# Kernel tuning notes

Measured on AMD Instinct MI355X. Metric: run time of the kernel, lower is better.

The kernel has to match this reference:

```python
import jax, jax.numpy as jnp
import numpy as np

D_MODEL = 1024
N_HEADS = 16
HEAD_DIM = D_MODEL // N_HEADS
ROPE_BASE = 10000.0


def setup_inputs() -> dict:
    key = jax.random.key(0)
    ks = jax.random.split(key, 9)
    s = 0.02
    inp = {
        "x": jax.random.normal(ks[0], (2, 2048, D_MODEL), dtype=jnp.float32),
        "Wq": jax.random.normal(ks[1], (D_MODEL, D_MODEL), dtype=jnp.float32) * s,
        "bq": jnp.zeros((D_MODEL,), dtype=jnp.float32),
        "Wk": jax.random.normal(ks[2], (D_MODEL, D_MODEL), dtype=jnp.float32) * s,
        "bk": jnp.zeros((D_MODEL,), dtype=jnp.float32),
        "Wv": jax.random.normal(ks[3], (D_MODEL, D_MODEL), dtype=jnp.float32) * s,
        "bv": jnp.zeros((D_MODEL,), dtype=jnp.float32),
        "Wo": jax.random.normal(ks[4], (D_MODEL, D_MODEL), dtype=jnp.float32) * s,
        "bo": jnp.zeros((D_MODEL,), dtype=jnp.float32),
    }
    return inp


def _rope_cos_sin(T, head_dim, dtype):
    inv_freq = 1.0 / (ROPE_BASE ** (jnp.arange(0, head_dim, 2, dtype=jnp.float32) / head_dim))
    pos = jnp.arange(T, dtype=jnp.float32)
    freqs = jnp.outer(pos, inv_freq)              # [T, head_dim/2]
    emb = jnp.concatenate([freqs, freqs], axis=-1)  # [T, head_dim]
    return jnp.cos(emb).astype(dtype), jnp.sin(emb).astype(dtype)


def _rotate_half(x):
    x1, x2 = jnp.split(x, 2, axis=-1)
    return jnp.concatenate([-x2, x1], axis=-1)


def reference(x, Wq, bq, Wk, bk, Wv, bv, Wo, bo):
    B, T, _ = x.shape
    H, Dh = N_HEADS, HEAD_DIM
    # projections (torch Linear: x @ W.T + b)
    q = (x @ Wq.T + bq).reshape(B, T, H, Dh).transpose(0, 2, 1, 3)  # [B,H,T,Dh]
    k = (x @ Wk.T + bk).reshape(B, T, H, Dh).transpose(0, 2, 1, 3)
    v = (x @ Wv.T + bv).reshape(B, T, H, Dh).transpose(0, 2, 1, 3)
    cos, sin = _rope_cos_sin(T, Dh, x.dtype)  # [T, Dh]
    cos = cos[None, None]
    sin = sin[None, None]
    q = q * cos + _rotate_half(q) * sin
    k = k * cos + _rotate_half(k) * sin
    scale = 1.0 / jnp.sqrt(jnp.asarray(Dh, dtype=x.dtype))
    attn = jnp.einsum("bhqd,bhkd->bhqk", q, k) * scale
    attn = jax.nn.softmax(attn, axis=-1)
    out = jnp.einsum("bhqk,bhkd->bhqd", attn, v)  # [B,H,T,Dh]
    out = out.transpose(0, 2, 1, 3).reshape(B, T, H * Dh)
    return out @ Wo.T + bo
```

## Files before the change

kernel.cpp:

```cpp
#include <hip/hip_runtime.h>
#include <hip/hip_bf16.h>
#include <cstdint>

#define D_MODEL 1024
#define NHEADS 16
#define HDIM 64
#define SEQ 2048
#define NBATCH 2
#define BT (NBATCH * SEQ)

typedef short bf16x8 __attribute__((ext_vector_type(8)));
typedef float f32x4 __attribute__((ext_vector_type(4)));
typedef unsigned short u16;
typedef unsigned int u32;

__device__ inline u16 f2bf(float f) {
    union { float f; u32 u; } x;
    x.f = f;
    u32 r = (x.u + 0x7fffu + ((x.u >> 16) & 1u)) >> 16;
    return (u16)r;
}

__device__ inline u32 pack2bf(float a, float b) {
    union { __hip_bfloat162 h; u32 u; } c;
    c.h = __float22bfloat162_rn(float2{a, b});
    return c.u;
}

__device__ inline float bf2f(u16 v) {
    union { u32 u; float f; } x;
    x.u = ((u32)v) << 16;
    return x.f;
}

__device__ inline void async_copy16(const u16* g, u16* l) {
    __builtin_amdgcn_global_load_lds((const __attribute__((address_space(1))) void*)g,
                                     (__attribute__((address_space(3))) void*)l, 16, 0, 0);
}

#define X4 (BT * D_MODEL / 4)
#define W4 (D_MODEL * D_MODEL / 4)
#define ROPE_N (SEQ * 32)

__global__ void prep_kernel(const float* __restrict__ x,
                            const float* __restrict__ wq, const float* __restrict__ wk,
                            const float* __restrict__ wv, const float* __restrict__ wo,
                            u16* __restrict__ xb,
                            u16* __restrict__ dq, u16* __restrict__ dk,
                            u16* __restrict__ dv, u16* __restrict__ dow,
                            float2* __restrict__ csT) {
    int idx = blockIdx.x * blockDim.x + threadIdx.x;
    if (idx < X4) {
        float4 v = ((const float4*)x)[idx];
        ushort4 o;
        o.x = f2bf(v.x); o.y = f2bf(v.y); o.z = f2bf(v.z); o.w = f2bf(v.w);
        ((ushort4*)xb)[idx] = o;
    } else if (idx < X4 + 4 * W4) {
        int j = idx - X4;
        int w = j >> 18, i = j & (W4 - 1);
        const float* s = (w == 0) ? wq : (w == 1) ? wk : (w == 2) ? wv : wo;
        u16* d = (w == 0) ? dq : (w == 1) ? dk : (w == 2) ? dv : dow;
        float4 v = ((const float4*)s)[i];
        ushort4 o;
        o.x = f2bf(v.x); o.y = f2bf(v.y); o.z = f2bf(v.z); o.w = f2bf(v.w);
        ((ushort4*)d)[i] = o;
    } else {
        int j = idx - (X4 + 4 * W4);
        if (j < ROPE_N) {
            int t = j >> 5, dm = j & 31;
            float invf = exp2f(-(float)dm * (13.287712379549449f / 32.0f));
            float ang = (float)t * invf;
            float s, c;
            sincosf(ang, &s, &c);
            csT[t * 32 + dm] = float2{c, s};
        }
    }
}

__device__ inline void gemm_tile_core(const u16* __restrict__ A, const u16* __restrict__ Bw,
                                      int blkM, int blkN,
                                      u16* Asmem, u16* Bsmem, f32x4 acc[4][4]) {
    const int tid = threadIdx.x;
    const int lane = tid & 63;
    const int wave = tid >> 6;
    const int waveM = wave >> 1, waveN = wave & 1;
    const int quad = lane >> 4, l16 = lane & 15;

    const int srow = tid >> 2;
    const int scol = (tid & 3) << 3;
    const u16* Ag0 = A + (size_t)(blkM * 128 + srow) * D_MODEL + scol;
    const u16* Ag1 = Ag0 + (size_t)64 * D_MODEL;
    const u16* Bg0 = Bw + (size_t)(blkN * 128 + srow) * D_MODEL + scol;
    const u16* Bg1 = Bg0 + (size_t)64 * D_MODEL;
    u16* Al0 = Asmem + srow * 32 + scol;
    u16* Al1 = Al0 + 64 * 32;
    u16* Bl0 = Bsmem + srow * 32 + scol;
    u16* Bl1 = Bl0 + 64 * 32;

    for (int k0 = 0; k0 < D_MODEL; k0 += 32) {
        __syncthreads();
        async_copy16(Ag0 + k0, Al0);
        async_copy16(Ag1 + k0, Al1);
        async_copy16(Bg0 + k0, Bl0);
        async_copy16(Bg1 + k0, Bl1);
        __syncthreads();
        bf16x8 af[4], bfr[4];
#pragma unroll
        for (int mt = 0; mt < 4; ++mt)
            af[mt] = *(const bf16x8*)&Asmem[(waveM * 64 + mt * 16 + l16) * 32 + quad * 8];
#pragma unroll
        for (int nt = 0; nt < 4; ++nt)
            bfr[nt] = *(const bf16x8*)&Bsmem[(waveN * 64 + nt * 16 + l16) * 32 + quad * 8];
#pragma unroll
        for (int mt = 0; mt < 4; ++mt)
#pragma unroll
            for (int nt = 0; nt < 4; ++nt)
                acc[mt][nt] = __builtin_amdgcn_mfma_f32_16x16x32_bf16(af[mt], bfr[nt], acc[mt][nt], 0, 0, 0);
    }
}

#define QSCALE 0.1803368801111204f
#define VPAD 132

__global__ __launch_bounds__(256) void gemm_qkv_kernel(
    const u16* __restrict__ xb,
    const u16* __restrict__ wqb, const u16* __restrict__ wkb, const u16* __restrict__ wvb,
    const float* __restrict__ bq, const float* __restrict__ bk, const float* __restrict__ bv,
    const float2* __restrict__ csT,
    u16* __restrict__ Qb, u16* __restrict__ Kb, u16* __restrict__ VTb) {
    __shared__ __align__(16) u16 smem[128 * VPAD];
    u16* Asmem = smem;
    u16* Bsmem = smem + 128 * 32;

    const int z = blockIdx.z;
    const u16* Bw = (z == 0) ? wqb : (z == 1) ? wkb : wvb;
    const float* bias = (z == 0) ? bq : (z == 1) ? bk : bv;

    f32x4 acc[4][4];
#pragma unroll
    for (int mt = 0; mt < 4; ++mt)
#pragma unroll
        for (int nt = 0; nt < 4; ++nt)
            acc[mt][nt] = (f32x4){0.f, 0.f, 0.f, 0.f};

    gemm_tile_core(xb, Bw, blockIdx.x, blockIdx.y, Asmem, Bsmem, acc);

    const int tid = threadIdx.x;
    const int lane = tid & 63, wave = tid >> 6;
    const int waveM = wave >> 1, waveN = wave & 1;
    const int quad = lane >> 4, l16 = lane & 15;
    const int gm0 = blockIdx.x * 128 + waveM * 64 + quad * 4;
    const int gn0 = blockIdx.y * 128 + waveN * 64 + l16;

    float bvv[4];
#pragma unroll
    for (int nt = 0; nt < 4; ++nt) bvv[nt] = bias[gn0 + nt * 16];
#pragma unroll
    for (int mt = 0; mt < 4; ++mt)
#pragma unroll
        for (int nt = 0; nt < 4; ++nt)
#pragma unroll
            for (int r = 0; r < 4; ++r) acc[mt][nt][r] += bvv[nt];

    if (z < 2) {
        u16* dst = (z == 0) ? Qb : Kb;
        const float post = (z == 0) ? QSCALE : 1.0f;
        const int h = 2 * blockIdx.y + waveN;
#pragma unroll
        for (int mt = 0; mt < 4; ++mt) {
#pragma unroll
            for (int r = 0; r < 4; ++r) {
                int gm = gm0 + mt * 16 + r;
                int t = gm & (SEQ - 1), b = gm >> 11;
                float2 cs0 = csT[t * 32 + l16];
                float2 cs1 = csT[t * 32 + 16 + l16];
                float a0 = acc[mt][0][r], a1 = acc[mt][1][r];
                float a2 = acc[mt][2][r], a3 = acc[mt][3][r];
                size_t base = ((size_t)(b * NHEADS + h) * SEQ + t) * HDIM;
                dst[base + l16]      = f2bf((a0 * cs0.x - a2 * cs0.y) * post);
                dst[base + l16 + 16] = f2bf((a1 * cs1.x - a3 * cs1.y) * post);
                dst[base + l16 + 32] = f2bf((a2 * cs0.x + a0 * cs0.y) * post);
                dst[base + l16 + 48] = f2bf((a3 * cs1.x + a1 * cs1.y) * post);
            }
        }
    } else {
        __syncthreads();
#pragma unroll
        for (int mt = 0; mt < 4; ++mt) {
            int t_local = waveM * 64 + mt * 16 + quad * 4;
#pragma unroll
            for (int nt = 0; nt < 4; ++nt) {
                int n_local = waveN * 64 + nt * 16 + l16;
                uint2 w;
                w.x = pack2bf(acc[mt][nt][0], acc[mt][nt][1]);
                w.y = pack2bf(acc[mt][nt][2], acc[mt][nt][3]);
                *(uint2*)&smem[n_local * VPAD + t_local] = w;
            }
        }
        __syncthreads();
        const int row = tid >> 1;
        const int hc = (tid & 1) * 64;
        const int n_g = blockIdx.y * 128 + row;
        const int h = n_g >> 6, d = n_g & 63;
        const int b = (blockIdx.x * 128) >> 11;
        const int t0 = ((blockIdx.x * 128) & (SEQ - 1)) + hc;
        u16* dst = &VTb[((size_t)(b * NHEADS + h) * HDIM + d) * SEQ + t0];
        const u16* src = &smem[row * VPAD + hc];
#pragma unroll
        for (int j = 0; j < 8; ++j)
            *(int4*)&dst[j * 8] = *(const int4*)&src[j * 8];
    }
}

#define LPAD 72

__global__ __launch_bounds__(256, 2) void flash_kernel(
    const u16* __restrict__ Qb, const u16* __restrict__ Kb, const u16* __restrict__ VTb,
    u16* __restrict__ Po0, u16* __restrict__ Po1, float* __restrict__ Ls) {
    __shared__ __align__(16) u16 Ps[4][64 * LPAD];

    const int tid = threadIdx.x;
    const int wave = tid >> 6, lane = tid & 63;
    const int quad = lane >> 4, l16 = lane & 15;
    const int bh = blockIdx.y;
    const int hf = blockIdx.z;
    const u16* Qh = Qb + (size_t)bh * SEQ * HDIM;
    const u16* Kh = Kb + (size_t)bh * SEQ * HDIM;
    const u16* Vh = VTb + (size_t)bh * HDIM * SEQ;
    const int qblk = blockIdx.x * 256 + wave * 64;
    u16* Pw = (u16*)Ps[wave];

    bf16x8 aq[4][2];
#pragma unroll
    for (int nt2 = 0; nt2 < 4; ++nt2)
#pragma unroll
        for (int ks = 0; ks < 2; ++ks)
            aq[nt2][ks] = *(const bf16x8*)&Qh[(qblk + nt2 * 16 + l16) * HDIM + ks * 32 + quad * 8];

    f32x4 o[4][4];
    float lsum[4] = {0.f, 0.f, 0.f, 0.f};
#pragma unroll
    for (int mt2 = 0; mt2 < 4; ++mt2)
#pragma unroll
        for (int nt = 0; nt < 4; ++nt) o[mt2][nt] = (f32x4){0.f, 0.f, 0.f, 0.f};

    const u16* Kp = Kh + (size_t)(hf * (SEQ / 2) + l16) * HDIM + quad * 8;
    const u16* Vp = Vh + (size_t)l16 * SEQ + hf * (SEQ / 2) + quad * 8;

    for (int it = 0; it < SEQ / 128; ++it) {
        f32x4 sacc[4][4];
#pragma unroll
        for (int mt = 0; mt < 4; ++mt)
#pragma unroll
            for (int nt2 = 0; nt2 < 4; ++nt2) sacc[mt][nt2] = (f32x4){0.f, 0.f, 0.f, 0.f};
#pragma unroll
        for (int ks = 0; ks < 2; ++ks) {
            bf16x8 kf[4];
#pragma unroll
            for (int mt = 0; mt < 4; ++mt)
                kf[mt] = *(const bf16x8*)&Kp[(size_t)(it * 64 + mt * 16) * HDIM + ks * 32];
#pragma unroll
            for (int mt = 0; mt < 4; ++mt)
#pragma unroll
                for (int nt2 = 0; nt2 < 4; ++nt2)
                    sacc[mt][nt2] = __builtin_amdgcn_mfma_f32_16x16x32_bf16(kf[mt], aq[nt2][ks], sacc[mt][nt2], 0, 0, 0);
        }

#pragma unroll
        for (int mt = 0; mt < 4; ++mt) {
#pragma unroll
            for (int nt2 = 0; nt2 < 4; ++nt2) {
                float p0 = __builtin_amdgcn_exp2f(sacc[mt][nt2][0]);
                float p1 = __builtin_amdgcn_exp2f(sacc[mt][nt2][1]);
                float p2 = __builtin_amdgcn_exp2f(sacc[mt][nt2][2]);
                float p3 = __builtin_amdgcn_exp2f(sacc[mt][nt2][3]);
                lsum[nt2] += (p0 + p1) + (p2 + p3);
                uint2 w;
                w.x = pack2bf(p0, p1);
                w.y = pack2bf(p2, p3);
                *(uint2*)&Pw[(nt2 * 16 + l16) * LPAD + mt * 16 + quad * 4] = w;
            }
        }

#pragma unroll
        for (int ks = 0; ks < 2; ++ks) {
            bf16x8 vf[4], pf[4];
#pragma unroll
            for (int nt = 0; nt < 4; ++nt)
                vf[nt] = *(const bf16x8*)&Vp[(size_t)(nt * 16) * SEQ + it * 64 + ks * 32];
#pragma unroll
            for (int mt2 = 0; mt2 < 4; ++mt2)
                pf[mt2] = *(const bf16x8*)&Pw[(mt2 * 16 + l16) * LPAD + ks * 32 + quad * 8];
#pragma unroll
            for (int mt2 = 0; mt2 < 4; ++mt2)
#pragma unroll
                for (int nt = 0; nt < 4; ++nt)
                    o[mt2][nt] = __builtin_amdgcn_mfma_f32_16x16x32_bf16(pf[mt2], vf[nt], o[mt2][nt], 0, 0, 0);
        }
    }

#pragma unroll
    for (int nt2 = 0; nt2 < 4; ++nt2) {
        lsum[nt2] += __shfl_xor(lsum[nt2], 16, 64);
        lsum[nt2] += __shfl_xor(lsum[nt2], 32, 64);
    }

    const int b = bh >> 4, h = bh & 15;
    u16* dst = hf ? Po1 : Po0;
#pragma unroll
    for (int mt2 = 0; mt2 < 4; ++mt2) {
#pragma unroll
        for (int nt = 0; nt < 4; ++nt) {
            int d = nt * 16 + l16;
#pragma unroll
            for (int r = 0; r < 4; ++r) {
                int q = qblk + mt2 * 16 + quad * 4 + r;
                dst[((size_t)(b * SEQ + q)) * D_MODEL + h * HDIM + d] = f2bf(o[mt2][nt][r]);
            }
        }
    }
    if (quad == 0) {
#pragma unroll
        for (int nt2 = 0; nt2 < 4; ++nt2) {
            int q = qblk + nt2 * 16 + l16;
            Ls[hf * (32 * SEQ) + bh * SEQ + q] = lsum[nt2];
        }
    }
}

__global__ __launch_bounds__(256) void gemm_out_kernel(
    const u16* __restrict__ Po0, const u16* __restrict__ Po1, const float* __restrict__ Ls,
    const u16* __restrict__ wob, const float* __restrict__ bo, float* __restrict__ dout) {
    __shared__ __align__(16) u16 Asmem[64 * 32];
    __shared__ __align__(16) u16 Bsmem[128 * 32];

    const int tid = threadIdx.x;
    const int lane = tid & 63, wave = tid >> 6;
    const int waveM = wave >> 1, waveN = wave & 1;
    const int quad = lane >> 4, l16 = lane & 15;

    f32x4 acc[2][4];
#pragma unroll
    for (int mt = 0; mt < 2; ++mt)
#pragma unroll
        for (int nt = 0; nt < 4; ++nt) acc[mt][nt] = (f32x4){0.f, 0.f, 0.f, 0.f};

    const int srow = tid >> 2;
    const int scol = (tid & 3) << 3;
    const int q = blockIdx.x * 64 + srow;
    const int b = q >> 11, t = q & (SEQ - 1);
    const size_t arow = (size_t)q * D_MODEL + scol;
    const u16* Bg0 = wob + (size_t)(blockIdx.y * 128 + srow) * D_MODEL + scol;
    const u16* Bg1 = Bg0 + (size_t)64 * D_MODEL;
    u16* Al = Asmem + srow * 32 + scol;
    u16* Bl0 = Bsmem + srow * 32 + scol;
    u16* Bl1 = Bl0 + 64 * 32;

    float rinvh[NHEADS];
    {
        const int bhq0 = b * NHEADS * SEQ + t;
#pragma unroll
        for (int h = 0; h < NHEADS; ++h) {
            int bhq = bhq0 + h * SEQ;
            rinvh[h] = 1.0f / (Ls[bhq] + Ls[32 * SEQ + bhq]);
        }
    }

    uint4 A0 = *(const uint4*)&Po0[arow];
    uint4 A1 = *(const uint4*)&Po1[arow];

    for (int k0 = 0; k0 < D_MODEL; k0 += 32) {
        __syncthreads();
        float rinv = rinvh[(k0 + scol) >> 6];
        const u16* p0 = (const u16*)&A0;
        const u16* p1 = (const u16*)&A1;
        uint4 wv;
        u32* wvp = (u32*)&wv;
#pragma unroll
        for (int j = 0; j < 4; ++j) {
            float s0 = (bf2f(p0[2 * j]) + bf2f(p1[2 * j])) * rinv;
            float s1 = (bf2f(p0[2 * j + 1]) + bf2f(p1[2 * j + 1])) * rinv;
            wvp[j] = pack2bf(s0, s1);
        }
        *(uint4*)Al = wv;
        async_copy16(Bg0 + k0, Bl0);
        async_copy16(Bg1 + k0, Bl1);
        if (k0 + 32 < D_MODEL) {
            A0 = *(const uint4*)&Po0[arow + k0 + 32];
            A1 = *(const uint4*)&Po1[arow + k0 + 32];
        }
        __syncthreads();
        bf16x8 af[2], bfr[4];
#pragma unroll
        for (int mt = 0; mt < 2; ++mt)
            af[mt] = *(const bf16x8*)&Asmem[(waveM * 32 + mt * 16 + l16) * 32 + quad * 8];
#pragma unroll
        for (int nt = 0; nt < 4; ++nt)
            bfr[nt] = *(const bf16x8*)&Bsmem[(waveN * 64 + nt * 16 + l16) * 32 + quad * 8];
#pragma unroll
        for (int mt = 0; mt < 2; ++mt)
#pragma unroll
            for (int nt = 0; nt < 4; ++nt)
                acc[mt][nt] = __builtin_amdgcn_mfma_f32_16x16x32_bf16(af[mt], bfr[nt], acc[mt][nt], 0, 0, 0);
    }

    const int gm0 = blockIdx.x * 64 + waveM * 32 + quad * 4;
    const int gn0 = blockIdx.y * 128 + waveN * 64 + l16;

    float bvv[4];
#pragma unroll
    for (int nt = 0; nt < 4; ++nt) bvv[nt] = bo[gn0 + nt * 16];
#pragma unroll
    for (int mt = 0; mt < 2; ++mt)
#pragma unroll
        for (int nt = 0; nt < 4; ++nt)
#pragma unroll
            for (int r = 0; r < 4; ++r)
                dout[(size_t)(gm0 + mt * 16 + r) * D_MODEL + gn0 + nt * 16] = acc[mt][nt][r] + bvv[nt];
}

extern "C" void kernel_launch(void* const* d_in, const int* in_sizes, int n_in,
                              void* d_out, int out_size, void* d_ws, size_t ws_size,
                              hipStream_t stream) {
    const float* x  = (const float*)d_in[0];
    const float* Wq = (const float*)d_in[1];
    const float* bq = (const float*)d_in[2];
    const float* Wk = (const float*)d_in[3];
    const float* bk = (const float*)d_in[4];
    const float* Wv = (const float*)d_in[5];
    const float* bv = (const float*)d_in[6];
    const float* Wo = (const float*)d_in[7];
    const float* bo = (const float*)d_in[8];
    float* dout = (float*)d_out;

    char* ws = (char*)d_ws;
    size_t off = 0;
    u16* xb  = (u16*)(ws + off); off += (size_t)BT * D_MODEL * 2;
    u16* wqb = (u16*)(ws + off); off += (size_t)D_MODEL * D_MODEL * 2;
    u16* wkb = (u16*)(ws + off); off += (size_t)D_MODEL * D_MODEL * 2;
    u16* wvb = (u16*)(ws + off); off += (size_t)D_MODEL * D_MODEL * 2;
    u16* wob = (u16*)(ws + off); off += (size_t)D_MODEL * D_MODEL * 2;
    u16* Qb  = (u16*)(ws + off); off += (size_t)BT * D_MODEL * 2;
    u16* Kb  = (u16*)(ws + off); off += (size_t)BT * D_MODEL * 2;
    u16* VTb = (u16*)(ws + off); off += (size_t)BT * D_MODEL * 2;
    u16* Po0 = (u16*)(ws + off); off += (size_t)BT * D_MODEL * 2;
    float2* csT = (float2*)(ws + off); off += (size_t)SEQ * 32 * 8;
    float* Ls   = (float*)(ws + off); off += (size_t)2 * 32 * SEQ * 4;
    u16* Po1 = xb;

    const int prepN = X4 + 4 * W4 + ROPE_N;
    prep_kernel<<<dim3((prepN + 255) / 256), 256, 0, stream>>>(
        x, Wq, Wk, Wv, Wo, xb, wqb, wkb, wvb, wob, csT);
    gemm_qkv_kernel<<<dim3(BT / 128, D_MODEL / 128, 3), 256, 0, stream>>>(
        xb, wqb, wkb, wvb, bq, bk, bv, csT, Qb, Kb, VTb);
    flash_kernel<<<dim3(SEQ / 256, NBATCH * NHEADS, 2), 256, 0, stream>>>(
        Qb, Kb, VTb, Po0, Po1, Ls);
    gemm_out_kernel<<<dim3(BT / 64, D_MODEL / 128), 256, 0, stream>>>(
        Po0, Po1, Ls, wob, bo, dout);
}
```

Baseline: 221.5 us.

## Stage K/V tiles in double-buffered shared memory with register prefetch

Each wave used to load K and V fragments straight from global memory, so the four waves of a block fetched the same tiles separately. Now the whole block loads each 64-key K and V^T tile once into padded LDS. Those loads are double-buffered, with a register prefetch two iterations ahead, so global latency overlaps with the MFMA work. The cost is more LDS per block (which may limit occupancy at 2 blocks/CU) and a __syncthreads per iteration.

```diff
diff --git a/kernel.cpp b/kernel.cpp
--- a/kernel.cpp
+++ b/kernel.cpp
@@ -217,6 +217,8 @@
 __global__ __launch_bounds__(256, 2) void flash_kernel(
     const u16* __restrict__ Qb, const u16* __restrict__ Kb, const u16* __restrict__ VTb,
     u16* __restrict__ Po0, u16* __restrict__ Po1, float* __restrict__ Ls) {
+    __shared__ __align__(16) u16 Ks[2][64 * LPAD];
+    __shared__ __align__(16) u16 VTs[2][64 * LPAD];
     __shared__ __align__(16) u16 Ps[4][64 * LPAD];
 
     const int tid = threadIdx.x;
@@ -225,8 +227,8 @@
     const int bh = blockIdx.y;
     const int hf = blockIdx.z;
     const u16* Qh = Qb + (size_t)bh * SEQ * HDIM;
-    const u16* Kh = Kb + (size_t)bh * SEQ * HDIM;
-    const u16* Vh = VTb + (size_t)bh * HDIM * SEQ;
+    const u16* Kh = Kb + ((size_t)bh * SEQ + hf * (SEQ / 2)) * HDIM;
+    const u16* Vh = VTb + (size_t)bh * HDIM * SEQ + hf * (SEQ / 2);
     const int qblk = blockIdx.x * 256 + wave * 64;
     u16* Pw = (u16*)Ps[wave];
 
@@ -244,10 +246,45 @@
 #pragma unroll
         for (int nt = 0; nt < 4; ++nt) o[mt2][nt] = (f32x4){0.f, 0.f, 0.f, 0.f};
 
-    const u16* Kp = Kh + (size_t)(hf * (SEQ / 2) + l16) * HDIM + quad * 8;
-    const u16* Vp = Vh + (size_t)l16 * SEQ + hf * (SEQ / 2) + quad * 8;
-
-    for (int it = 0; it < SEQ / 128; ++it) {
+    const int lr = tid >> 2;
+    const int lc = (tid & 3) * 16;
+    const u16* Kg = Kh + (size_t)lr * HDIM + lc;
+    const u16* Vg = Vh + (size_t)lr * SEQ + lc;
+    const int sidx = lr * LPAD + lc;
+
+    uint4 ka, kc, va, vc;
+    ka = *(const uint4*)&Kg[0];
+    kc = *(const uint4*)&Kg[8];
+    va = *(const uint4*)&Vg[0];
+    vc = *(const uint4*)&Vg[8];
+    *(uint4*)&Ks[0][sidx] = ka;
+    *(uint4*)&Ks[0][sidx + 8] = kc;
+    *(uint4*)&VTs[0][sidx] = va;
+    *(uint4*)&VTs[0][sidx + 8] = vc;
+    ka = *(const uint4*)&Kg[(size_t)64 * HDIM];
+    kc = *(const uint4*)&Kg[(size_t)64 * HDIM + 8];
+    va = *(const uint4*)&Vg[64];
+    vc = *(const uint4*)&Vg[64 + 8];
+    __syncthreads();
+
+#pragma unroll 2
+    for (int it = 0; it < 16; ++it) {
+        const int cur = it & 1;
+        if (it < 15) {
+            *(uint4*)&Ks[cur ^ 1][sidx] = ka;
+            *(uint4*)&Ks[cur ^ 1][sidx + 8] = kc;
+            *(uint4*)&VTs[cur ^ 1][sidx] = va;
+            *(uint4*)&VTs[cur ^ 1][sidx + 8] = vc;
+        }
+        if (it < 14) {
+            ka = *(const uint4*)&Kg[(size_t)(it + 2) * 64 * HDIM];
+            kc = *(const uint4*)&Kg[(size_t)(it + 2) * 64 * HDIM + 8];
+            va = *(const uint4*)&Vg[(it + 2) * 64];
+            vc = *(const uint4*)&Vg[(it + 2) * 64 + 8];
+        }
+        const u16* Ksc = Ks[cur];
+        const u16* Vsc = VTs[cur];
+
         f32x4 sacc[4][4];
 #pragma unroll
         for (int mt = 0; mt < 4; ++mt)
@@ -258,7 +295,7 @@
             bf16x8 kf[4];
 #pragma unroll
             for (int mt = 0; mt < 4; ++mt)
-                kf[mt] = *(const bf16x8*)&Kp[(size_t)(it * 64 + mt * 16) * HDIM + ks * 32];
+                kf[mt] = *(const bf16x8*)&Ksc[(mt * 16 + l16) * LPAD + ks * 32 + quad * 8];
 #pragma unroll
             for (int mt = 0; mt < 4; ++mt)
 #pragma unroll
@@ -284,19 +321,20 @@
 
 #pragma unroll
         for (int ks = 0; ks < 2; ++ks) {
-            bf16x8 vf[4], pf[4];
-#pragma unroll
-            for (int nt = 0; nt < 4; ++nt)
-                vf[nt] = *(const bf16x8*)&Vp[(size_t)(nt * 16) * SEQ + it * 64 + ks * 32];
+            bf16x8 pf[4], vf[4];
 #pragma unroll
             for (int mt2 = 0; mt2 < 4; ++mt2)
                 pf[mt2] = *(const bf16x8*)&Pw[(mt2 * 16 + l16) * LPAD + ks * 32 + quad * 8];
 #pragma unroll
+            for (int nt = 0; nt < 4; ++nt)
+                vf[nt] = *(const bf16x8*)&Vsc[(nt * 16 + l16) * LPAD + ks * 32 + quad * 8];
+#pragma unroll
             for (int mt2 = 0; mt2 < 4; ++mt2)
 #pragma unroll
                 for (int nt = 0; nt < 4; ++nt)
                     o[mt2][nt] = __builtin_amdgcn_mfma_f32_16x16x32_bf16(pf[mt2], vf[nt], o[mt2][nt], 0, 0, 0);
         }
+        __syncthreads();
     }
 
 #pragma unroll
```

Result: faster. 202.1 us (-8.8%).
